# Kernel tuning notes

Hardware: AMD Instinct MI355X
Metric: run time of the kernel (lower is better)

The kernel has to match this reference:

```python
import jax, jax.numpy as jnp
import numpy as np

TOP_K = 4
NUM_EXPERTS = 32
HIDDEN = 2880


def setup_inputs() -> dict:
    key = jax.random.key(0)
    k1, k2, k3 = jax.random.split(key, 3)
    hidden_states = jax.random.normal(k1, (4, 4096, HIDDEN), dtype=jnp.float32)
    # Router params: weight [num_experts, hidden], bias [num_experts]
    weight = jax.random.normal(k2, (NUM_EXPERTS, HIDDEN), dtype=jnp.float32) * (1.0 / np.sqrt(HIDDEN))
    bias = jax.random.normal(k3, (NUM_EXPERTS,), dtype=jnp.float32) * 0.01
    return {"hidden_states": hidden_states, "weight": weight, "bias": bias}


def reference(hidden_states, weight, bias):
    # Flatten tokens: [T, H]
    h = hidden_states.reshape(-1, hidden_states.shape[-1])
    # Router logits: F.linear(h, W, b) = h @ W.T + b -> [T, E]
    router_logits = jnp.einsum("th,eh->te", h, weight) + bias
    # Top-k over experts
    router_top_value, router_indices = jax.lax.top_k(router_logits, TOP_K)  # [T, K]
    # Softmax over the k selected logits (in float32, cast back)
    router_top_value = jax.nn.softmax(router_top_value.astype(jnp.float32), axis=-1).astype(router_logits.dtype)
    # Scatter into dense zero scores: [T, E]
    router_scores = jnp.zeros_like(router_logits)
    t_idx = jnp.arange(h.shape[0])[:, None]  # [T, 1] broadcast against [T, K]
    router_scores = router_scores.at[t_idx, router_indices].set(router_top_value)
    return router_scores, router_indices
```

## Files before the change

### kernel.cpp

```cpp
#include <hip/hip_runtime.h>
#include <math.h>

#define NE 32
#define HID 2880
#define NSTEP 90
#define TT 64
#define THREADS 256
#define WSB_BYTES (3 * NSTEP * 2 * 64 * 16)

typedef short bf16x8 __attribute__((ext_vector_type(8)));
typedef float f32x4 __attribute__((ext_vector_type(4)));

union FragU { uint4 q; bf16x8 v; };

#define GLL(gsrc, ldst)                                                        \
  __builtin_amdgcn_global_load_lds(                                            \
      (const __attribute__((address_space(1))) unsigned int*)(gsrc),           \
      (__attribute__((address_space(3))) unsigned int*)(ldst), 16, 0, 0)

__global__ void __launch_bounds__(256) wsplit_kernel(
    const float* __restrict__ w, unsigned int* __restrict__ wsB)
{
  const int gid = blockIdx.x * 256 + threadIdx.x;
  const int s  = gid >> 7;
  const int tl = (gid >> 6) & 1;
  const int l  = gid & 63;

  const float* src = w + (size_t)(tl * 16 + (l & 15)) * HID + s * 32 + ((l >> 4) * 8);
  float4 xa = *(const float4*)src;
  float4 xb = *(const float4*)(src + 4);
  float x[8] = {xa.x, xa.y, xa.z, xa.w, xb.x, xb.y, xb.z, xb.w};

  unsigned int u0[8], u1[8], u2[8];
#pragma unroll
  for (int j = 0; j < 8; ++j) {
    unsigned int ux = __float_as_uint(x[j]);
    u0[j] = ux & 0xFFFF0000u;
    float r1 = x[j] - __uint_as_float(u0[j]);
    u1[j] = __float_as_uint(r1) & 0xFFFF0000u;
    float r2 = r1 - __uint_as_float(u1[j]);
    u2[j] = __float_as_uint(r2);
  }

  uint4* dst = (uint4*)wsB;
  uint4 d;
  d.x = __builtin_amdgcn_perm(u0[1], u0[0], 0x07060302u);
  d.y = __builtin_amdgcn_perm(u0[3], u0[2], 0x07060302u);
  d.z = __builtin_amdgcn_perm(u0[5], u0[4], 0x07060302u);
  d.w = __builtin_amdgcn_perm(u0[7], u0[6], 0x07060302u);
  dst[((0 * NSTEP + s) * 2 + tl) * 64 + l] = d;
  d.x = __builtin_amdgcn_perm(u1[1], u1[0], 0x07060302u);
  d.y = __builtin_amdgcn_perm(u1[3], u1[2], 0x07060302u);
  d.z = __builtin_amdgcn_perm(u1[5], u1[4], 0x07060302u);
  d.w = __builtin_amdgcn_perm(u1[7], u1[6], 0x07060302u);
  dst[((1 * NSTEP + s) * 2 + tl) * 64 + l] = d;
  d.x = __builtin_amdgcn_perm(u2[1], u2[0], 0x07060302u);
  d.y = __builtin_amdgcn_perm(u2[3], u2[2], 0x07060302u);
  d.z = __builtin_amdgcn_perm(u2[5], u2[4], 0x07060302u);
  d.w = __builtin_amdgcn_perm(u2[7], u2[6], 0x07060302u);
  dst[((2 * NSTEP + s) * 2 + tl) * 64 + l] = d;
}

__global__ void __launch_bounds__(THREADS) router_mfma(
    const float* __restrict__ hs,
    const unsigned int* __restrict__ wsB,
    float* __restrict__ wsp,
    int T, int KQ, int ntg)
{
  __shared__ float hbuf[2][4096];
  __shared__ float wbuf[2][3072];

  const int tid = threadIdx.x;
  const int wv  = __builtin_amdgcn_readfirstlane(tid >> 6);
  const int l   = tid & 63;
  const int q   = l >> 4;
  const int r15 = l & 15;
  const int tg  = blockIdx.x % ntg;
  const int kq  = blockIdx.x / ntg;
  const int t0  = tg * TT;

  int nsteps, s0;
  if (KQ == 4) { nsteps = (kq == 0) ? 24 : 22; s0 = (kq == 0) ? 0 : (2 + 22 * kq); }
  else         { nsteps = (kq == 0) ? 46 : 44; s0 = (kq == 0) ? 0 : 46; }
  const int nchunk = nsteps >> 1;

  int goffH[4];
#pragma unroll
  for (int i = 0; i < 4; ++i) {
    int f = tid + 256 * i;
    int row = f >> 4;
    int G = (f & 15) ^ (row & 15);
    goffH[i] = row * HID + G * 4;
  }
  int goffW[3];
#pragma unroll
  for (int i = 0; i < 3; ++i) {
    int j = tid + 256 * i;
    int f = j >> 6, e = j & 63;
    int p = f >> 2, sl = (f >> 1) & 1, t = f & 1;
    goffW[i] = ((p * 2 * NSTEP + sl * 2 + t) * 64 + e);
  }

  const int hrowb = (wv * 16 + r15) * 256;

  f32x4 acc0 = {0.f, 0.f, 0.f, 0.f};
  f32x4 acc1 = {0.f, 0.f, 0.f, 0.f};

  const float* hbase = hs + (size_t)t0 * HID + s0 * 32;
  const uint4* wsb4 = (const uint4*)wsB;

#define STAGE(j)                                                               \
  {                                                                            \
    const float* hn = hbase + (j) * 64;                                        \
    char* hb_n = (char*)&hbuf[(j) & 1][0];                                     \
    char* wb_n = (char*)&wbuf[(j) & 1][0];                                     \
    _Pragma("unroll")                                                          \
    for (int i = 0; i < 4; ++i)                                                \
      GLL(hn + goffH[i], hb_n + (tid + 256 * i) * 16);                         \
    _Pragma("unroll")                                                          \
    for (int i = 0; i < 3; ++i)                                                \
      GLL(wsb4 + goffW[i] + (size_t)(s0 + 2 * (j)) * 128,                      \
          wb_n + (tid + 256 * i) * 16);                                        \
  }

  STAGE(0);

#pragma clang loop unroll(disable)
  for (int c = 0; c < nchunk; ++c) {
    __builtin_amdgcn_s_barrier();

    if (c + 1 < nchunk) {
      STAGE(c + 1);
      asm volatile("s_waitcnt vmcnt(7)" ::: "memory");
    } else {
      asm volatile("s_waitcnt vmcnt(0)" ::: "memory");
    }
    __builtin_amdgcn_sched_barrier(0);
    __builtin_amdgcn_s_barrier();
    __builtin_amdgcn_sched_barrier(0);

    const char* cb = (const char*)&hbuf[c & 1][0];
    const uint4* wl = (const uint4*)&wbuf[c & 1][0];

#pragma unroll
    for (int sl = 0; sl < 2; ++sl) {
      FragU W00, W01, W10, W11, W20, W21;
      W00.q = wl[(0 + sl * 2 + 0) * 64 + l];
      W01.q = wl[(0 + sl * 2 + 1) * 64 + l];
      W10.q = wl[(4 + sl * 2 + 0) * 64 + l];
      W11.q = wl[(4 + sl * 2 + 1) * 64 + l];
      W20.q = wl[(8 + sl * 2 + 0) * 64 + l];
      W21.q = wl[(8 + sl * 2 + 1) * 64 + l];

      float4 h0 = *(const float4*)(cb + hrowb + (((sl * 8 + 2 * q + 0) ^ r15) << 4));
      float4 h1 = *(const float4*)(cb + hrowb + (((sl * 8 + 2 * q + 1) ^ r15) << 4));
      float x[8] = {h0.x, h0.y, h0.z, h0.w, h1.x, h1.y, h1.z, h1.w};

      unsigned int u0[8], u1[8], u2[8];
#pragma unroll
      for (int j = 0; j < 8; ++j) {
        unsigned int ux = __float_as_uint(x[j]);
        u0[j] = ux & 0xFFFF0000u;
        float r1 = x[j] - __uint_as_float(u0[j]);
        u1[j] = __float_as_uint(r1) & 0xFFFF0000u;
        float r2 = r1 - __uint_as_float(u1[j]);
        u2[j] = __float_as_uint(r2);
      }
      FragU A0, A1, A2;
      A0.q.x = __builtin_amdgcn_perm(u0[1], u0[0], 0x07060302u);
      A0.q.y = __builtin_amdgcn_perm(u0[3], u0[2], 0x07060302u);
      A0.q.z = __builtin_amdgcn_perm(u0[5], u0[4], 0x07060302u);
      A0.q.w = __builtin_amdgcn_perm(u0[7], u0[6], 0x07060302u);
      A1.q.x = __builtin_amdgcn_perm(u1[1], u1[0], 0x07060302u);
      A1.q.y = __builtin_amdgcn_perm(u1[3], u1[2], 0x07060302u);
      A1.q.z = __builtin_amdgcn_perm(u1[5], u1[4], 0x07060302u);
      A1.q.w = __builtin_amdgcn_perm(u1[7], u1[6], 0x07060302u);
      A2.q.x = __builtin_amdgcn_perm(u2[1], u2[0], 0x07060302u);
      A2.q.y = __builtin_amdgcn_perm(u2[3], u2[2], 0x07060302u);
      A2.q.z = __builtin_amdgcn_perm(u2[5], u2[4], 0x07060302u);
      A2.q.w = __builtin_amdgcn_perm(u2[7], u2[6], 0x07060302u);

      acc0 = __builtin_amdgcn_mfma_f32_16x16x32_bf16(A0.v, W00.v, acc0, 0, 0, 0);
      acc0 = __builtin_amdgcn_mfma_f32_16x16x32_bf16(A0.v, W10.v, acc0, 0, 0, 0);
      acc0 = __builtin_amdgcn_mfma_f32_16x16x32_bf16(A1.v, W00.v, acc0, 0, 0, 0);
      acc0 = __builtin_amdgcn_mfma_f32_16x16x32_bf16(A1.v, W10.v, acc0, 0, 0, 0);
      acc0 = __builtin_amdgcn_mfma_f32_16x16x32_bf16(A0.v, W20.v, acc0, 0, 0, 0);
      acc0 = __builtin_amdgcn_mfma_f32_16x16x32_bf16(A2.v, W00.v, acc0, 0, 0, 0);
      acc1 = __builtin_amdgcn_mfma_f32_16x16x32_bf16(A0.v, W01.v, acc1, 0, 0, 0);
      acc1 = __builtin_amdgcn_mfma_f32_16x16x32_bf16(A0.v, W11.v, acc1, 0, 0, 0);
      acc1 = __builtin_amdgcn_mfma_f32_16x16x32_bf16(A1.v, W01.v, acc1, 0, 0, 0);
      acc1 = __builtin_amdgcn_mfma_f32_16x16x32_bf16(A1.v, W11.v, acc1, 0, 0, 0);
      acc1 = __builtin_amdgcn_mfma_f32_16x16x32_bf16(A0.v, W21.v, acc1, 0, 0, 0);
      acc1 = __builtin_amdgcn_mfma_f32_16x16x32_bf16(A2.v, W01.v, acc1, 0, 0, 0);
    }
  }

  float* dst = wsp + ((size_t)kq * T + t0 + wv * 16) * NE;
#pragma unroll
  for (int r = 0; r < 4; ++r) {
    dst[(q * 4 + r) * NE + r15]      = acc0[r];
    dst[(q * 4 + r) * NE + 16 + r15] = acc1[r];
  }
}

__global__ void __launch_bounds__(256) router_topk(
    const float* __restrict__ wsp, const float* __restrict__ bias,
    float* __restrict__ out, int T, int KQ)
{
  const int tok = blockIdx.x * 256 + threadIdx.x;

  float lg[NE];
#pragma unroll
  for (int e = 0; e < NE; e += 4) {
    float4 bb = *(const float4*)(bias + e);
    lg[e] = bb.x; lg[e+1] = bb.y; lg[e+2] = bb.z; lg[e+3] = bb.w;
  }
  for (int qq = 0; qq < KQ; ++qq) {
    const float* p = wsp + ((size_t)qq * T + tok) * NE;
#pragma unroll
    for (int e = 0; e < NE; e += 4) {
      float4 v = *(const float4*)(p + e);
      lg[e] += v.x; lg[e+1] += v.y; lg[e+2] += v.z; lg[e+3] += v.w;
    }
  }

  float tv[4]; int ti[4];
#pragma unroll
  for (int kk = 0; kk < 4; ++kk) {
    float m = -INFINITY; int mi = 0;
#pragma unroll
    for (int e = 0; e < NE; ++e) {
      bool gt = lg[e] > m;
      m  = gt ? lg[e] : m;
      mi = gt ? e : mi;
    }
    tv[kk] = m; ti[kk] = mi;
#pragma unroll
    for (int e = 0; e < NE; ++e)
      lg[e] = (e == mi) ? -INFINITY : lg[e];
  }

  float e1 = __expf(tv[1] - tv[0]);
  float e2 = __expf(tv[2] - tv[0]);
  float e3 = __expf(tv[3] - tv[0]);
  float inv = 1.0f / (1.0f + e1 + e2 + e3);
  float pr[4] = {inv, e1 * inv, e2 * inv, e3 * inv};

  float* orow = out + (size_t)tok * NE;
#pragma unroll
  for (int g = 0; g < 8; ++g) {
    float4 v;
    float* vp = (float*)&v;
#pragma unroll
    for (int cb = 0; cb < 4; ++cb) {
      int e = g * 4 + cb;
      float xx = 0.f;
      xx = (e == ti[0]) ? pr[0] : xx;
      xx = (e == ti[1]) ? pr[1] : xx;
      xx = (e == ti[2]) ? pr[2] : xx;
      xx = (e == ti[3]) ? pr[3] : xx;
      vp[cb] = xx;
    }
    *(float4*)(orow + g * 4) = v;
  }
  float* oidx = out + (size_t)T * NE + (size_t)tok * 4;
  float4 iv;
  iv.x = (float)ti[0]; iv.y = (float)ti[1]; iv.z = (float)ti[2]; iv.w = (float)ti[3];
  *(float4*)oidx = iv;
}

extern "C" void kernel_launch(void* const* d_in, const int* in_sizes, int n_in,
                              void* d_out, int out_size, void* d_ws, size_t ws_size,
                              hipStream_t stream) {
  const float* hs   = (const float*)d_in[0];
  const float* w    = (const float*)d_in[1];
  const float* bias = (const float*)d_in[2];
  float* out        = (float*)d_out;

  unsigned int* wsB = (unsigned int*)d_ws;
  float* wsp        = (float*)((char*)d_ws + WSB_BYTES);

  const int T   = in_sizes[0] / HID;
  const int ntg = T / TT;

  const size_t per_kq = (size_t)T * NE * 4;
  const int KQ = (ws_size >= WSB_BYTES + 4 * per_kq) ? 4 : 2;

  hipLaunchKernelGGL(wsplit_kernel, dim3(45), dim3(256), 0, stream, w, wsB);
  hipLaunchKernelGGL(router_mfma, dim3(ntg * KQ), dim3(THREADS), 0, stream,
                     hs, wsB, wsp, T, KQ, ntg);
  hipLaunchKernelGGL(router_topk, dim3(T / 256), dim3(256), 0, stream,
                     wsp, bias, out, T, KQ);
}
```

Baseline: 50.37 us.

## Switch router GEMM to triple-buffered single-step LDS pipeline with prefetch depth two

The router MFMA loop now stages one K-step (32 columns) per iteration instead of two, into three rotating LDS buffers. Two stages are kept in flight, with the vmcnt waits adjusted to match. This is meant to hide more global-load latency in this memory-bound kernel, and it shrinks LDS per block, which may allow more resident blocks. The cost is twice as many loop iterations and barriers, plus an extra dummy weight load for half the threads.

```diff
diff --git a/kernel.cpp b/kernel.cpp
--- a/kernel.cpp
+++ b/kernel.cpp
@@ -67,8 +67,8 @@
     float* __restrict__ wsp,
     int T, int KQ, int ntg)
 {
-  __shared__ float hbuf[2][4096];
-  __shared__ float wbuf[2][3072];
+  __shared__ float hbuf[3][2048];
+  __shared__ float wbuf[3][2048];
 
   const int tid = threadIdx.x;
   const int wv  = __builtin_amdgcn_readfirstlane(tid >> 6);
@@ -82,26 +82,29 @@
   int nsteps, s0;
   if (KQ == 4) { nsteps = (kq == 0) ? 24 : 22; s0 = (kq == 0) ? 0 : (2 + 22 * kq); }
   else         { nsteps = (kq == 0) ? 46 : 44; s0 = (kq == 0) ? 0 : 46; }
-  const int nchunk = nsteps >> 1;
-
-  int goffH[4];
-#pragma unroll
-  for (int i = 0; i < 4; ++i) {
+  const int nchunk = nsteps;
+
+  int goffH[2];
+#pragma unroll
+  for (int i = 0; i < 2; ++i) {
     int f = tid + 256 * i;
-    int row = f >> 4;
-    int G = (f & 15) ^ (row & 15);
+    int row = f >> 3;
+    int G = (f & 7) ^ (row & 7);
     goffH[i] = row * HID + G * 4;
   }
-  int goffW[3];
-#pragma unroll
-  for (int i = 0; i < 3; ++i) {
-    int j = tid + 256 * i;
-    int f = j >> 6, e = j & 63;
-    int p = f >> 2, sl = (f >> 1) & 1, t = f & 1;
-    goffW[i] = ((p * 2 * NSTEP + sl * 2 + t) * 64 + e);
-  }
-
-  const int hrowb = (wv * 16 + r15) * 256;
+  int goffW[2];
+  {
+    int f0 = tid >> 6, e0 = tid & 63;
+    goffW[0] = (((f0 >> 1) * NSTEP * 2) + (f0 & 1)) * 64 + e0;
+    if (tid < 128) {
+      int f1 = 4 + (tid >> 6), e1 = tid & 63;
+      goffW[1] = (((f1 >> 1) * NSTEP * 2) + (f1 & 1)) * 64 + e1;
+    } else {
+      goffW[1] = 0;
+    }
+  }
+
+  const int hrowb = (wv * 16 + r15) * 128;
 
   f32x4 acc0 = {0.f, 0.f, 0.f, 0.f};
   f32x4 acc1 = {0.f, 0.f, 0.f, 0.f};
@@ -111,27 +114,28 @@
 
 #define STAGE(j)                                                               \
   {                                                                            \
-    const float* hn = hbase + (j) * 64;                                        \
-    char* hb_n = (char*)&hbuf[(j) & 1][0];                                     \
-    char* wb_n = (char*)&wbuf[(j) & 1][0];                                     \
-    _Pragma("unroll")                                                          \
-    for (int i = 0; i < 4; ++i)                                                \
-      GLL(hn + goffH[i], hb_n + (tid + 256 * i) * 16);                         \
-    _Pragma("unroll")                                                          \
-    for (int i = 0; i < 3; ++i)                                                \
-      GLL(wsb4 + goffW[i] + (size_t)(s0 + 2 * (j)) * 128,                      \
-          wb_n + (tid + 256 * i) * 16);                                        \
+    const int b = (j) % 3;                                                     \
+    const float* hn = hbase + (j) * 32;                                        \
+    char* hb_n = (char*)&hbuf[b][0];                                           \
+    char* wb_n = (char*)&wbuf[b][0];                                           \
+    GLL(hn + goffH[0], hb_n + tid * 16);                                       \
+    GLL(hn + goffH[1], hb_n + (tid + 256) * 16);                               \
+    GLL(wsb4 + goffW[0] + (size_t)(s0 + (j)) * 128, wb_n + tid * 16);          \
+    GLL(wsb4 + goffW[1] + (size_t)(s0 + (j)) * 128, wb_n + (tid + 256) * 16);  \
   }
 
   STAGE(0);
+  STAGE(1);
 
 #pragma clang loop unroll(disable)
   for (int c = 0; c < nchunk; ++c) {
     __builtin_amdgcn_s_barrier();
 
-    if (c + 1 < nchunk) {
-      STAGE(c + 1);
-      asm volatile("s_waitcnt vmcnt(7)" ::: "memory");
+    if (c + 2 < nchunk) {
+      STAGE(c + 2);
+      asm volatile("s_waitcnt vmcnt(8)" ::: "memory");
+    } else if (c + 1 < nchunk) {
+      asm volatile("s_waitcnt vmcnt(4)" ::: "memory");
     } else {
       asm volatile("s_waitcnt vmcnt(0)" ::: "memory");
     }
@@ -139,60 +143,58 @@
     __builtin_amdgcn_s_barrier();
     __builtin_amdgcn_sched_barrier(0);
 
-    const char* cb = (const char*)&hbuf[c & 1][0];
-    const uint4* wl = (const uint4*)&wbuf[c & 1][0];
-
-#pragma unroll
-    for (int sl = 0; sl < 2; ++sl) {
-      FragU W00, W01, W10, W11, W20, W21;
-      W00.q = wl[(0 + sl * 2 + 0) * 64 + l];
-      W01.q = wl[(0 + sl * 2 + 1) * 64 + l];
-      W10.q = wl[(4 + sl * 2 + 0) * 64 + l];
-      W11.q = wl[(4 + sl * 2 + 1) * 64 + l];
-      W20.q = wl[(8 + sl * 2 + 0) * 64 + l];
-      W21.q = wl[(8 + sl * 2 + 1) * 64 + l];
-
-      float4 h0 = *(const float4*)(cb + hrowb + (((sl * 8 + 2 * q + 0) ^ r15) << 4));
-      float4 h1 = *(const float4*)(cb + hrowb + (((sl * 8 + 2 * q + 1) ^ r15) << 4));
-      float x[8] = {h0.x, h0.y, h0.z, h0.w, h1.x, h1.y, h1.z, h1.w};
-
-      unsigned int u0[8], u1[8], u2[8];
-#pragma unroll
-      for (int j = 0; j < 8; ++j) {
-        unsigned int ux = __float_as_uint(x[j]);
-        u0[j] = ux & 0xFFFF0000u;
-        float r1 = x[j] - __uint_as_float(u0[j]);
-        u1[j] = __float_as_uint(r1) & 0xFFFF0000u;
-        float r2 = r1 - __uint_as_float(u1[j]);
-        u2[j] = __float_as_uint(r2);
-      }
-      FragU A0, A1, A2;
-      A0.q.x = __builtin_amdgcn_perm(u0[1], u0[0], 0x07060302u);
-      A0.q.y = __builtin_amdgcn_perm(u0[3], u0[2], 0x07060302u);
-      A0.q.z = __builtin_amdgcn_perm(u0[5], u0[4], 0x07060302u);
-      A0.q.w = __builtin_amdgcn_perm(u0[7], u0[6], 0x07060302u);
-      A1.q.x = __builtin_amdgcn_perm(u1[1], u1[0], 0x07060302u);
-      A1.q.y = __builtin_amdgcn_perm(u1[3], u1[2], 0x07060302u);
-      A1.q.z = __builtin_amdgcn_perm(u1[5], u1[4], 0x07060302u);
-      A1.q.w = __builtin_amdgcn_perm(u1[7], u1[6], 0x07060302u);
-      A2.q.x = __builtin_amdgcn_perm(u2[1], u2[0], 0x07060302u);
-      A2.q.y = __builtin_amdgcn_perm(u2[3], u2[2], 0x07060302u);
-      A2.q.z = __builtin_amdgcn_perm(u2[5], u2[4], 0x07060302u);
-      A2.q.w = __builtin_amdgcn_perm(u2[7], u2[6], 0x07060302u);
-
-      acc0 = __builtin_amdgcn_mfma_f32_16x16x32_bf16(A0.v, W00.v, acc0, 0, 0, 0);
-      acc0 = __builtin_amdgcn_mfma_f32_16x16x32_bf16(A0.v, W10.v, acc0, 0, 0, 0);
-      acc0 = __builtin_amdgcn_mfma_f32_16x16x32_bf16(A1.v, W00.v, acc0, 0, 0, 0);
-      acc0 = __builtin_amdgcn_mfma_f32_16x16x32_bf16(A1.v, W10.v, acc0, 0, 0, 0);
-      acc0 = __builtin_amdgcn_mfma_f32_16x16x32_bf16(A0.v, W20.v, acc0, 0, 0, 0);
-      acc0 = __builtin_amdgcn_mfma_f32_16x16x32_bf16(A2.v, W00.v, acc0, 0, 0, 0);
-      acc1 = __builtin_amdgcn_mfma_f32_16x16x32_bf16(A0.v, W01.v, acc1, 0, 0, 0);
-      acc1 = __builtin_amdgcn_mfma_f32_16x16x32_bf16(A0.v, W11.v, acc1, 0, 0, 0);
-      acc1 = __builtin_amdgcn_mfma_f32_16x16x32_bf16(A1.v, W01.v, acc1, 0, 0, 0);
-      acc1 = __builtin_amdgcn_mfma_f32_16x16x32_bf16(A1.v, W11.v, acc1, 0, 0, 0);
-      acc1 = __builtin_amdgcn_mfma_f32_16x16x32_bf16(A0.v, W21.v, acc1, 0, 0, 0);
-      acc1 = __builtin_amdgcn_mfma_f32_16x16x32_bf16(A2.v, W01.v, acc1, 0, 0, 0);
-    }
+    const int b = c % 3;
+    const char* cb = (const char*)&hbuf[b][0];
+    const uint4* wl = (const uint4*)&wbuf[b][0];
+
+    FragU W00, W01, W10, W11, W20, W21;
+    W00.q = wl[0 * 64 + l];
+    W01.q = wl[1 * 64 + l];
+    W10.q = wl[2 * 64 + l];
+    W11.q = wl[3 * 64 + l];
+    W20.q = wl[4 * 64 + l];
+    W21.q = wl[5 * 64 + l];
+
+    float4 h0 = *(const float4*)(cb + hrowb + (((2 * q + 0) ^ (r15 & 7)) << 4));
+    float4 h1 = *(const float4*)(cb + hrowb + (((2 * q + 1) ^ (r15 & 7)) << 4));
+    float x[8] = {h0.x, h0.y, h0.z, h0.w, h1.x, h1.y, h1.z, h1.w};
+
+    unsigned int u0[8], u1[8], u2[8];
+#pragma unroll
+    for (int j = 0; j < 8; ++j) {
+      unsigned int ux = __float_as_uint(x[j]);
+      u0[j] = ux & 0xFFFF0000u;
+      float r1 = x[j] - __uint_as_float(u0[j]);
+      u1[j] = __float_as_uint(r1) & 0xFFFF0000u;
+      float r2 = r1 - __uint_as_float(u1[j]);
+      u2[j] = __float_as_uint(r2);
+    }
+    FragU A0, A1, A2;
+    A0.q.x = __builtin_amdgcn_perm(u0[1], u0[0], 0x07060302u);
+    A0.q.y = __builtin_amdgcn_perm(u0[3], u0[2], 0x07060302u);
+    A0.q.z = __builtin_amdgcn_perm(u0[5], u0[4], 0x07060302u);
+    A0.q.w = __builtin_amdgcn_perm(u0[7], u0[6], 0x07060302u);
+    A1.q.x = __builtin_amdgcn_perm(u1[1], u1[0], 0x07060302u);
+    A1.q.y = __builtin_amdgcn_perm(u1[3], u1[2], 0x07060302u);
+    A1.q.z = __builtin_amdgcn_perm(u1[5], u1[4], 0x07060302u);
+    A1.q.w = __builtin_amdgcn_perm(u1[7], u1[6], 0x07060302u);
+    A2.q.x = __builtin_amdgcn_perm(u2[1], u2[0], 0x07060302u);
+    A2.q.y = __builtin_amdgcn_perm(u2[3], u2[2], 0x07060302u);
+    A2.q.z = __builtin_amdgcn_perm(u2[5], u2[4], 0x07060302u);
+    A2.q.w = __builtin_amdgcn_perm(u2[7], u2[6], 0x07060302u);
+
+    acc0 = __builtin_amdgcn_mfma_f32_16x16x32_bf16(A0.v, W00.v, acc0, 0, 0, 0);
+    acc0 = __builtin_amdgcn_mfma_f32_16x16x32_bf16(A0.v, W10.v, acc0, 0, 0, 0);
+    acc0 = __builtin_amdgcn_mfma_f32_16x16x32_bf16(A1.v, W00.v, acc0, 0, 0, 0);
+    acc0 = __builtin_amdgcn_mfma_f32_16x16x32_bf16(A1.v, W10.v, acc0, 0, 0, 0);
+    acc0 = __builtin_amdgcn_mfma_f32_16x16x32_bf16(A0.v, W20.v, acc0, 0, 0, 0);
+    acc0 = __builtin_amdgcn_mfma_f32_16x16x32_bf16(A2.v, W00.v, acc0, 0, 0, 0);
+    acc1 = __builtin_amdgcn_mfma_f32_16x16x32_bf16(A0.v, W01.v, acc1, 0, 0, 0);
+    acc1 = __builtin_amdgcn_mfma_f32_16x16x32_bf16(A0.v, W11.v, acc1, 0, 0, 0);
+    acc1 = __builtin_amdgcn_mfma_f32_16x16x32_bf16(A1.v, W01.v, acc1, 0, 0, 0);
+    acc1 = __builtin_amdgcn_mfma_f32_16x16x32_bf16(A1.v, W11.v, acc1, 0, 0, 0);
+    acc1 = __builtin_amdgcn_mfma_f32_16x16x32_bf16(A0.v, W21.v, acc1, 0, 0, 0);
+    acc1 = __builtin_amdgcn_mfma_f32_16x16x32_bf16(A2.v, W01.v, acc1, 0, 0, 0);
   }
 
   float* dst = wsp + ((size_t)kq * T + t0 + wv * 16) * NE;
```

Result: slower. 56.33 us (+11.8%).
